# Performance work log

Measured on AMD Instinct MI355X. Metric: run time of the kernel, lower is better.

The kernel has to match this reference:

```python
import jax, jax.numpy as jnp
import numpy as np

B, T, D = 4, 1024, 256
H, DK, C = 8, 32, 16  # n_heads, d_key, pos-encoder hidden units
DV = D // H
NEG = -1e15
EPS_SM = 1e-5
EPS_LN = 1e-5
SLOPE = 0.01  # LeakyReLU default


def setup_inputs() -> dict:
    key = jax.random.key(0)
    ks = jax.random.split(key, 16)
    s = 0.05
    x = jax.random.normal(ks[0], (B, T, D), jnp.float32)
    src_mask = jax.random.randint(ks[1], (B, T, T), 0, 2).astype(bool)
    rel_dists = jax.random.uniform(ks[2], (B, 1, T, T), jnp.float32)
    Wq = jax.random.normal(ks[3], (H, DK, D), jnp.float32) * s
    Wk = jax.random.normal(ks[4], (H, DK, D), jnp.float32) * s
    Wv = jax.random.normal(ks[5], (H, DV, D), jnp.float32) * s
    pw1 = jax.random.normal(ks[6], (H, C), jnp.float32) * s
    pb1 = jax.random.normal(ks[7], (H, C), jnp.float32) * s
    pw2 = jax.random.normal(ks[8], (H, C), jnp.float32) * s
    pb2 = jax.random.normal(ks[9], (H,), jnp.float32) * s
    Wo = jax.random.normal(ks[10], (D, D), jnp.float32) * s
    bo = jax.random.normal(ks[11], (D,), jnp.float32) * s
    Wf = jax.random.normal(ks[12], (D, D), jnp.float32) * s
    bf = jax.random.normal(ks[13], (D,), jnp.float32) * s
    g1 = jnp.ones((D,), jnp.float32)
    beta1 = jnp.zeros((D,), jnp.float32)
    g2 = jnp.ones((D,), jnp.float32)
    beta2 = jnp.zeros((D,), jnp.float32)
    return dict(x=x, src_mask=src_mask, rel_dists=rel_dists, Wq=Wq, Wk=Wk, Wv=Wv,
                pw1=pw1, pb1=pb1, pw2=pw2, pb2=pb2, Wo=Wo, bo=bo, Wf=Wf, bf=bf,
                g1=g1, beta1=beta1, g2=g2, beta2=beta2)


def _l2norm(v):
    # F.normalize(p=2, dim=-1): v / max(||v||, 1e-12)
    n = jnp.sqrt(jnp.sum(v * v, axis=-1, keepdims=True))
    return v / jnp.maximum(n, 1e-12)


def _lrelu(h):
    return jnp.where(h >= 0, h, SLOPE * h)


def _pos_bias(d, pw1, pb1, pw2, pb2):
    # d: [B,T,T]; per-head 1x1-conv MLP applied elementwise.
    # Loop over the tiny channel dim (16) to avoid a [B,H,T,T,C] intermediate.
    bias = jnp.broadcast_to(pb2[None, :, None, None], (d.shape[0], pw1.shape[0], d.shape[1], d.shape[2]))
    for c in range(pw1.shape[1]):
        h = d[:, None] * pw1[None, :, c, None, None] + pb1[None, :, c, None, None]
        bias = bias + pw2[None, :, c, None, None] * _lrelu(h)
    return bias  # [B,H,T,T]


def _layer_norm(v, g, b):
    mu = jnp.mean(v, axis=-1, keepdims=True)
    var = jnp.mean((v - mu) ** 2, axis=-1, keepdims=True)
    return (v - mu) * jax.lax.rsqrt(var + EPS_LN) * g + b


def reference(x, src_mask, rel_dists, Wq, Wk, Wv, pw1, pb1, pw2, pb2,
              Wo, bo, Wf, bf, g1, beta1, g2, beta2):
    # cosine-normalized multi-head attention (all heads batched)
    q = _l2norm(jnp.einsum('btd,hkd->bhtk', x, Wq))
    k = _l2norm(jnp.einsum('bsd,hkd->bhsk', x, Wk))
    v = jnp.einsum('bsd,hvd->bhsv', x, Wv)
    logits = jnp.einsum('bhtk,bhsk->bhts', q, k)
    logits = logits - _pos_bias(rel_dists[:, 0], pw1, pb1, pw2, pb2)
    logits = jnp.where(src_mask[:, None], NEG, logits)
    # custom softmax: exp / (sum + 1e-5) (handles all-padded rows)
    z = jnp.exp(logits)
    attn = z / (jnp.sum(z, axis=-1, keepdims=True) + EPS_SM)
    heads = jnp.einsum('bhts,bhsv->bhtv', attn, v)
    y = heads.transpose(0, 2, 1, 3).reshape(x.shape[0], x.shape[1], -1)  # concat heads
    y = y @ Wo.T + bo
    # residual + LN + FFN (dropout is identity in eval mode)
    zz = _layer_norm(x + y, g1, beta1)
    z_ff = _lrelu(zz @ Wf.T + bf)
    return _layer_norm(zz + z_ff, g2, beta2)
```

## Files before the change

### kernel.cpp

```cpp
#include <hip/hip_runtime.h>
#include <math.h>

#define Bc 4
#define Tc 1024
#define Dc 256
#define Hc 8
#define Cc 16
#define LUTN 256
#define LOG2E 1.4426950408889634f

typedef __attribute__((ext_vector_type(8))) short short8;
typedef __attribute__((ext_vector_type(4))) float f32x4;

__device__ __forceinline__ unsigned bf16u(float x) {
    unsigned u = __float_as_uint(x);
    return (u + 0x7FFFu + ((u >> 16) & 1u)) >> 16;
}
__device__ __forceinline__ unsigned pk2(float lo, float hi) {
    return bf16u(lo) | (bf16u(hi) << 16);
}
__device__ __forceinline__ unsigned pk2t(float lo, float hi) {
    return __builtin_amdgcn_perm(__float_as_uint(hi), __float_as_uint(lo), 0x07060302u);
}
__device__ __forceinline__ float upk(unsigned v) { return __uint_as_float(v << 16); }
__device__ __forceinline__ float upkh(unsigned v) { return __uint_as_float(v & 0xffff0000u); }
__device__ __forceinline__ float fexp2(float x) { return __builtin_amdgcn_exp2f(x); }

__global__ __launch_bounds__(256) void prep_all(
    const float* __restrict__ x,
    const float* __restrict__ Wq, const float* __restrict__ Wk,
    const float* __restrict__ Wv, const float* __restrict__ Wo,
    const float* __restrict__ Wf,
    const float* __restrict__ rel, const int* __restrict__ msk,
    const float* __restrict__ pw1, const float* __restrict__ pb1,
    const float* __restrict__ pw2, const float* __restrict__ pb2,
    ushort* __restrict__ Xc, ushort* __restrict__ Wqkvc,
    ushort* __restrict__ Woc, ushort* __restrict__ Wfc,
    ushort* __restrict__ Dm, ushort* __restrict__ LUTb)
{
    const int bid = blockIdx.x;
    if (bid < 1344) {
        const int e = (bid * 256 + threadIdx.x) * 4;
        const float* src; ushort* dst; int off;
        if (e < 1048576)      { src = x;  dst = Xc;             off = e; }
        else if (e < 1114112) { src = Wq; dst = Wqkvc;          off = e - 1048576; }
        else if (e < 1179648) { src = Wk; dst = Wqkvc + 65536;  off = e - 1114112; }
        else if (e < 1245184) { src = Wv; dst = Wqkvc + 131072; off = e - 1179648; }
        else if (e < 1310720) { src = Wo; dst = Woc;            off = e - 1245184; }
        else                  { src = Wf; dst = Wfc;            off = e - 1310720; }
        float4 v = *(const float4*)(src + off);
        uint2 p; p.x = pk2(v.x, v.y); p.y = pk2(v.z, v.w);
        *(uint2*)(dst + off) = p;
    } else if (bid < 3392) {
        const size_t e = ((size_t)(bid - 1344) * 256 + threadIdx.x) * 8;
        float4 d0 = *(const float4*)(rel + e);
        float4 d1 = *(const float4*)(rel + e + 4);
        int4 m0 = *(const int4*)(msk + e);
        int4 m1 = *(const int4*)(msk + e + 4);
        uint4 o;
        o.x = pk2(m0.x ? -1.f : d0.x, m0.y ? -1.f : d0.y);
        o.y = pk2(m0.z ? -1.f : d0.z, m0.w ? -1.f : d0.w);
        o.z = pk2(m1.x ? -1.f : d1.x, m1.y ? -1.f : d1.y);
        o.w = pk2(m1.z ? -1.f : d1.z, m1.w ? -1.f : d1.w);
        *(uint4*)(Dm + e) = o;
    } else {
        const int bin = threadIdx.x;
        const float d0 = bin * (1.f / LUTN), d1 = (bin + 1) * (1.f / LUTN);
        for (int h = 0; h < Hc; ++h) {
            float y0 = pb2[h], y1 = pb2[h];
#pragma unroll
            for (int c = 0; c < Cc; ++c) {
                float w1 = pw1[h * Cc + c], b1 = pb1[h * Cc + c], w2 = pw2[h * Cc + c];
                float h0 = fmaf(w1, d0, b1), h1 = fmaf(w1, d1, b1);
                y0 = fmaf(w2, h0 >= 0.f ? h0 : 0.01f * h0, y0);
                y1 = fmaf(w2, h1 >= 0.f ? h1 : 0.01f * h1, y1);
            }
            float a = (y1 - y0) * (float)LUTN;
            float b = y0 - a * d0;
            LUTb[(h >> 2) * 2048 + bin * 8 + (h & 3) * 2]     = (ushort)bf16u(a * LOG2E);
            LUTb[(h >> 2) * 2048 + bin * 8 + (h & 3) * 2 + 1] = (ushort)bf16u(b * LOG2E);
        }
    }
}

__global__ __launch_bounds__(256) void qkv_direct(
    const ushort* __restrict__ Xc, const ushort* __restrict__ Wqkv,
    ushort* __restrict__ Qb, ushort* __restrict__ Kb, ushort* __restrict__ Vt)
{
    const int tid = threadIdx.x;
    const int w = tid >> 6;
    const int l = tid & 63;
    const int u = l & 15, g = l >> 4;
    const int rbase = blockIdx.x * 16;
    const int cb = (blockIdx.y * 4 + w) * 64;
    const int mat = cb >> 8;
    const int fcb = cb & 255;

    f32x4 acc[4];
#pragma unroll
    for (int nt = 0; nt < 4; ++nt) acc[nt] = (f32x4){0.f, 0.f, 0.f, 0.f};

    const ushort* arow = Xc + (size_t)(rbase + u) * 256 + g * 8;
#pragma unroll 2
    for (int k0 = 0; k0 < 256; k0 += 32) {
        short8 af = *(const short8*)(arow + k0);
#pragma unroll
        for (int nt = 0; nt < 4; ++nt) {
            short8 bfr = *(const short8*)(Wqkv + (size_t)(cb + nt * 16 + u) * 256 + k0 + g * 8);
            acc[nt] = __builtin_amdgcn_mfma_f32_16x16x32_bf16(af, bfr, acc[nt], 0, 0, 0);
        }
    }

    if (mat < 2) {
        ushort* Out = (mat == 0) ? Qb : Kb;
        const float post = (mat == 0) ? LOG2E : 1.f;
#pragma unroll
        for (int hp = 0; hp < 2; ++hp) {
            const int head = (fcb >> 5) + hp;
#pragma unroll
            for (int reg = 0; reg < 4; ++reg) {
                float ss = acc[2 * hp][reg] * acc[2 * hp][reg]
                         + acc[2 * hp + 1][reg] * acc[2 * hp + 1][reg];
                ss += __shfl_xor(ss, 1, 64);
                ss += __shfl_xor(ss, 2, 64);
                ss += __shfl_xor(ss, 4, 64);
                ss += __shfl_xor(ss, 8, 64);
                float scn = post / fmaxf(sqrtf(ss), 1e-12f);
                const int t = rbase + 4 * g + reg;
                const int bb = t >> 10, tt = t & 1023;
                const size_t base = ((size_t)(bb * 8 + head) * Tc + tt) * 32;
                Out[base + u]      = (ushort)bf16u(acc[2 * hp][reg] * scn);
                Out[base + 16 + u] = (ushort)bf16u(acc[2 * hp + 1][reg] * scn);
            }
        }
    } else {
#pragma unroll
        for (int nt = 0; nt < 4; ++nt) {
            const int head = (fcb >> 5) + (nt >> 1);
            const int vt = nt & 1;
#pragma unroll
            for (int reg = 0; reg < 4; ++reg) {
                const int s = rbase + 4 * g + reg;
                const int bb = s >> 10, ss = s & 1023;
                const int bh = bb * 8 + head;
                Vt[(((size_t)bh * 32 + (ss >> 5)) * 2 + vt) * 512 + u * 32 + (ss & 31)] =
                    (ushort)bf16u(acc[nt][reg]);
            }
        }
    }
}

__global__ __launch_bounds__(512) void attn_mfma(
    const ushort* __restrict__ Qb, const ushort* __restrict__ Kb,
    const ushort* __restrict__ Vt,
    const ushort* __restrict__ Dm, const ushort* __restrict__ LUTb,
    ushort* __restrict__ Yb)
{
    const int tid = threadIdx.x;
    const int w = tid >> 6;
    const int l = tid & 63;
    const int u = l & 15;
    const int g = l >> 4;
    const int t0 = blockIdx.x * 16;
    const int b = blockIdx.y;
    const int hg = blockIdx.z;

    __shared__ __align__(16) ushort lut_s[2048];
    __shared__ __align__(16) unsigned plds[8 * 320];
    __shared__ __align__(16) ushort comb[8 * 16 * 136];
    __shared__ float rs_s[8 * 64];

    *(uint2*)(lut_s + tid * 4) = *(const uint2*)(LUTb + hg * 2048 + tid * 4);

    const int bh0 = b * 8 + hg * 4;
    short8 qf[4];
#pragma unroll
    for (int hi = 0; hi < 4; ++hi)
        qf[hi] = *(const short8*)(Qb + (((size_t)(bh0 + hi) * Tc + t0 + u) * 32 + g * 8));

    const short8 ones = (short8){0x3F80, 0x3F80, 0x3F80, 0x3F80,
                                 0x3F80, 0x3F80, 0x3F80, 0x3F80};

    f32x4 oacc[4][2];
    f32x4 rsacc[4];
#pragma unroll
    for (int hi = 0; hi < 4; ++hi) {
        oacc[hi][0] = (f32x4){0.f, 0.f, 0.f, 0.f};
        oacc[hi][1] = (f32x4){0.f, 0.f, 0.f, 0.f};
        rsacc[hi]   = (f32x4){0.f, 0.f, 0.f, 0.f};
    }

    unsigned* pwb = plds + w * 320;
    const size_t dbase = (size_t)b * Tc * Tc;

    __syncthreads();

    const int s_begin = w * 128;
#pragma unroll
    for (int ch = 0; ch < 4; ++ch) {
        const int sc = s_begin + ch * 32;
        float dA[4], dB[4];
#pragma unroll
        for (int reg = 0; reg < 4; ++reg) {
            const int t = t0 + 4 * g + reg;
            unsigned dm = *(const unsigned*)(Dm + dbase + (size_t)t * Tc + sc + 2 * u);
            dA[reg] = upk(dm);
            dB[reg] = upkh(dm);
        }
        float biasA[4][4], biasB[4][4];
#pragma unroll
        for (int reg = 0; reg < 4; ++reg) {
            int iA = (int)(dA[reg] * (float)LUTN);
            int iB = (int)(dB[reg] * (float)LUTN);
            iA = iA < 0 ? 0 : (iA > LUTN - 1 ? LUTN - 1 : iA);
            iB = iB < 0 ? 0 : (iB > LUTN - 1 ? LUTN - 1 : iB);
            uint4 wA = *(const uint4*)(lut_s + iA * 8);
            uint4 wB = *(const uint4*)(lut_s + iB * 8);
            biasA[reg][0] = fmaf(upk(wA.x), dA[reg], upkh(wA.x));
            biasA[reg][1] = fmaf(upk(wA.y), dA[reg], upkh(wA.y));
            biasA[reg][2] = fmaf(upk(wA.z), dA[reg], upkh(wA.z));
            biasA[reg][3] = fmaf(upk(wA.w), dA[reg], upkh(wA.w));
            biasB[reg][0] = fmaf(upk(wB.x), dB[reg], upkh(wB.x));
            biasB[reg][1] = fmaf(upk(wB.y), dB[reg], upkh(wB.y));
            biasB[reg][2] = fmaf(upk(wB.z), dB[reg], upkh(wB.z));
            biasB[reg][3] = fmaf(upk(wB.w), dB[reg], upkh(wB.w));
        }
#pragma unroll
        for (int hi = 0; hi < 4; ++hi) {
            const size_t kb = ((size_t)(bh0 + hi) * Tc + sc + 2 * u) * 32 + g * 8;
            short8 kfA = *(const short8*)(Kb + kb);
            short8 kfB = *(const short8*)(Kb + kb + 32);
            const f32x4 z4 = (f32x4){0.f, 0.f, 0.f, 0.f};
            f32x4 sA = __builtin_amdgcn_mfma_f32_16x16x32_bf16(qf[hi], kfA, z4, 0, 0, 0);
            f32x4 sB = __builtin_amdgcn_mfma_f32_16x16x32_bf16(qf[hi], kfB, z4, 0, 0, 0);
#pragma unroll
            for (int reg = 0; reg < 4; ++reg) {
                float zA = (dA[reg] < 0.f) ? 0.f : fexp2(sA[reg] - biasA[reg][hi]);
                float zB = (dB[reg] < 0.f) ? 0.f : fexp2(sB[reg] - biasB[reg][hi]);
                pwb[(4 * g + reg) * 20 + u] = pk2t(zA, zB);
            }
            short8 pf = *(const short8*)((const char*)pwb + u * 80 + g * 16);
            const ushort* vb = Vt + ((size_t)(bh0 + hi) * 32 + (sc >> 5)) * 1024;
            short8 vf0 = *(const short8*)(vb + u * 32 + g * 8);
            short8 vf1 = *(const short8*)(vb + 512 + u * 32 + g * 8);
            oacc[hi][0] = __builtin_amdgcn_mfma_f32_16x16x32_bf16(pf, vf0, oacc[hi][0], 0, 0, 0);
            oacc[hi][1] = __builtin_amdgcn_mfma_f32_16x16x32_bf16(pf, vf1, oacc[hi][1], 0, 0, 0);
            rsacc[hi]   = __builtin_amdgcn_mfma_f32_16x16x32_bf16(pf, ones, rsacc[hi], 0, 0, 0);
        }
    }

#pragma unroll
    for (int hi = 0; hi < 4; ++hi)
        if (u == 0) {
#pragma unroll
            for (int reg = 0; reg < 4; ++reg)
                rs_s[(w * 4 + hi) * 16 + 4 * g + reg] = rsacc[hi][reg];
        }
#pragma unroll
    for (int hi = 0; hi < 4; ++hi)
#pragma unroll
        for (int vt = 0; vt < 2; ++vt)
#pragma unroll
            for (int reg = 0; reg < 4; ++reg)
                comb[w * 2176 + (4 * g + reg) * 136 + hi * 32 + vt * 16 + u] =
                    (ushort)(__float_as_uint(oacc[hi][vt][reg]) >> 16);
    __syncthreads();

    const int tl = tid >> 5;
    const int f0 = (tid & 31) * 4;
    const int hl = f0 >> 5;
    float rstot = 0.f;
#pragma unroll
    for (int ww = 0; ww < 8; ++ww) rstot += rs_s[(ww * 4 + hl) * 16 + tl];
    float inv = 1.f / (rstot + 1e-5f);
    float o[4] = {0.f, 0.f, 0.f, 0.f};
#pragma unroll
    for (int ww = 0; ww < 8; ++ww) {
        uint2 pv = *(const uint2*)&comb[ww * 2176 + tl * 136 + f0];
        o[0] += upk(pv.x); o[1] += upkh(pv.x);
        o[2] += upk(pv.y); o[3] += upkh(pv.y);
    }
    uint2 pw;
    pw.x = pk2(o[0] * inv, o[1] * inv);
    pw.y = pk2(o[2] * inv, o[3] * inv);
    *(uint2*)(Yb + ((size_t)b * Tc + t0 + tl) * Dc + hg * 128 + f0) = pw;
}

__global__ __launch_bounds__(256) void gemm_ln(
    const ushort* __restrict__ A, const ushort* __restrict__ W,
    const float* __restrict__ bias,
    const float* __restrict__ resF, const ushort* __restrict__ resB,
    const float* __restrict__ gam, const float* __restrict__ bet,
    float* __restrict__ outF, ushort* __restrict__ outB, int act)
{
    const int tid = threadIdx.x;
    const int w = tid >> 6;
    const int l = tid & 63;
    const int u = l & 15, g = l >> 4;
    const int rbase = blockIdx.x * 16;

    __shared__ float red1[64], red2[64];

    f32x4 acc[4];
#pragma unroll
    for (int nt = 0; nt < 4; ++nt) acc[nt] = (f32x4){0.f, 0.f, 0.f, 0.f};

    const ushort* arow = A + (size_t)(rbase + u) * 256 + g * 8;
#pragma unroll 2
    for (int k0 = 0; k0 < 256; k0 += 32) {
        short8 af = *(const short8*)(arow + k0);
#pragma unroll
        for (int nt = 0; nt < 4; ++nt) {
            short8 bfr = *(const short8*)(W + (size_t)(w * 64 + nt * 16 + u) * 256 + k0 + g * 8);
            acc[nt] = __builtin_amdgcn_mfma_f32_16x16x32_bf16(af, bfr, acc[nt], 0, 0, 0);
        }
    }

    float bv[4];
#pragma unroll
    for (int nt = 0; nt < 4; ++nt) bv[nt] = bias[w * 64 + nt * 16 + u];

    float sv[4][4];
#pragma unroll
    for (int reg = 0; reg < 4; ++reg) {
        const int row = rbase + 4 * g + reg;
        float s1 = 0.f, s2 = 0.f;
#pragma unroll
        for (int nt = 0; nt < 4; ++nt) {
            const int col = w * 64 + nt * 16 + u;
            float v = acc[nt][reg] + bv[nt];
            if (act) v = v >= 0.f ? v : 0.01f * v;
            float res = resF ? resF[(size_t)row * 256 + col]
                             : upk((unsigned)resB[(size_t)row * 256 + col]);
            float s = v + res;
            sv[reg][nt] = s;
            s1 += s;
            s2 = fmaf(s, s, s2);
        }
        s1 += __shfl_xor(s1, 1, 64); s2 += __shfl_xor(s2, 1, 64);
        s1 += __shfl_xor(s1, 2, 64); s2 += __shfl_xor(s2, 2, 64);
        s1 += __shfl_xor(s1, 4, 64); s2 += __shfl_xor(s2, 4, 64);
        s1 += __shfl_xor(s1, 8, 64); s2 += __shfl_xor(s2, 8, 64);
        if (u == 0) { red1[w * 16 + 4 * g + reg] = s1; red2[w * 16 + 4 * g + reg] = s2; }
    }
    __syncthreads();

    float gv[4], btv[4];
#pragma unroll
    for (int nt = 0; nt < 4; ++nt) {
        gv[nt]  = gam[w * 64 + nt * 16 + u];
        btv[nt] = bet[w * 64 + nt * 16 + u];
    }
#pragma unroll
    for (int reg = 0; reg < 4; ++reg) {
        const int row = rbase + 4 * g + reg;
        const int rl = 4 * g + reg;
        float S1 = red1[rl] + red1[16 + rl] + red1[32 + rl] + red1[48 + rl];
        float S2 = red2[rl] + red2[16 + rl] + red2[32 + rl] + red2[48 + rl];
        float mu = S1 * (1.f / 256.f);
        float var = S2 * (1.f / 256.f) - mu * mu;
        float rsig = rsqrtf(var + 1e-5f);
#pragma unroll
        for (int nt = 0; nt < 4; ++nt) {
            const int col = w * 64 + nt * 16 + u;
            float o = (sv[reg][nt] - mu) * rsig * gv[nt] + btv[nt];
            if (outF) outF[(size_t)row * 256 + col] = o;
            else      outB[(size_t)row * 256 + col] = (ushort)bf16u(o);
        }
    }
}

extern "C" void kernel_launch(void* const* d_in, const int* in_sizes, int n_in,
                              void* d_out, int out_size, void* d_ws, size_t ws_size,
                              hipStream_t stream) {
    const float* x    = (const float*)d_in[0];
    const int*   mask = (const int*)d_in[1];
    const float* rel  = (const float*)d_in[2];
    const float* Wq   = (const float*)d_in[3];
    const float* Wk   = (const float*)d_in[4];
    const float* Wv   = (const float*)d_in[5];
    const float* pw1  = (const float*)d_in[6];
    const float* pb1  = (const float*)d_in[7];
    const float* pw2  = (const float*)d_in[8];
    const float* pb2  = (const float*)d_in[9];
    const float* Wo   = (const float*)d_in[10];
    const float* bo   = (const float*)d_in[11];
    const float* Wf   = (const float*)d_in[12];
    const float* bf   = (const float*)d_in[13];
    const float* g1   = (const float*)d_in[14];
    const float* be1  = (const float*)d_in[15];
    const float* g2   = (const float*)d_in[16];
    const float* be2  = (const float*)d_in[17];
    float* out = (float*)d_out;

    char* wsb = (char*)d_ws;
    ushort* Xc    = (ushort*)(wsb);
    ushort* Qb    = (ushort*)(wsb + (size_t)( 2 << 20));
    ushort* Kb    = (ushort*)(wsb + (size_t)( 4 << 20));
    ushort* Vt    = (ushort*)(wsb + (size_t)( 6 << 20));
    ushort* Yb    = (ushort*)(wsb + (size_t)( 8 << 20));
    ushort* Wqkvc = (ushort*)(wsb + (size_t)(10 << 20));
    ushort* Woc   = (ushort*)(wsb + (size_t)(10 << 20) + (512 << 10));
    ushort* Wfc   = (ushort*)(wsb + (size_t)(10 << 20) + (768 << 10));
    ushort* LUTb  = (ushort*)(wsb + (size_t)(11 << 20));
    ushort* ZZb   = (ushort*)(wsb + (size_t)(12 << 20));
    ushort* Dm    = (ushort*)(wsb + (size_t)(16 << 20));

    prep_all<<<3393, 256, 0, stream>>>(x, Wq, Wk, Wv, Wo, Wf, rel, mask,
                                       pw1, pb1, pw2, pb2,
                                       Xc, Wqkvc, Woc, Wfc, Dm, LUTb);
    qkv_direct<<<dim3(256, 3), 256, 0, stream>>>(Xc, Wqkvc, Qb, Kb, Vt);
    attn_mfma<<<dim3(64, 4, 2), 512, 0, stream>>>(Qb, Kb, Vt, Dm, LUTb, Yb);
    gemm_ln<<<256, 256, 0, stream>>>(Yb, Woc, bo, x, nullptr, g1, be1,
                                     nullptr, ZZb, 0);
    gemm_ln<<<256, 256, 0, stream>>>(ZZb, Wfc, bf, nullptr, ZZb, g2, be2,
                                     out, nullptr, 1);
}
```

Baseline: 177.8 us.

## Co-schedule mask/distance packing with QKV GEMM and widen LN GEMM blocks

Splits the prep kernel so that only the bf16 casts run first, and folds the rel-dist/mask packing and LUT build into the QKV projection launch as extra blocks. The bandwidth-heavy mask conversion then overlaps with the QKV MFMA work instead of running serially before it. The gemm_ln kernels move to 512 threads with 8 waves each covering 32 columns, which adds parallelism per row tile and changes the LayerNorm reduction to sum over 8 wave partials. The cost is more waves competing for the same row data in each block.

```diff
diff --git a/kernel.cpp b/kernel.cpp
--- a/kernel.cpp
+++ b/kernel.cpp
@@ -26,33 +26,57 @@
 __device__ __forceinline__ float upkh(unsigned v) { return __uint_as_float(v & 0xffff0000u); }
 __device__ __forceinline__ float fexp2(float x) { return __builtin_amdgcn_exp2f(x); }
 
-__global__ __launch_bounds__(256) void prep_all(
+__global__ __launch_bounds__(256) void prep_cast(
     const float* __restrict__ x,
     const float* __restrict__ Wq, const float* __restrict__ Wk,
     const float* __restrict__ Wv, const float* __restrict__ Wo,
     const float* __restrict__ Wf,
+    ushort* __restrict__ Xc, ushort* __restrict__ Wqkvc,
+    ushort* __restrict__ Woc, ushort* __restrict__ Wfc)
+{
+    const int e = (blockIdx.x * 256 + threadIdx.x) * 4;
+    const float* src; ushort* dst; int off;
+    if (e < 1048576)      { src = x;  dst = Xc;             off = e; }
+    else if (e < 1114112) { src = Wq; dst = Wqkvc;          off = e - 1048576; }
+    else if (e < 1179648) { src = Wk; dst = Wqkvc + 65536;  off = e - 1114112; }
+    else if (e < 1245184) { src = Wv; dst = Wqkvc + 131072; off = e - 1179648; }
+    else if (e < 1310720) { src = Wo; dst = Woc;            off = e - 1245184; }
+    else                  { src = Wf; dst = Wfc;            off = e - 1310720; }
+    float4 v = *(const float4*)(src + off);
+    uint2 p; p.x = pk2(v.x, v.y); p.y = pk2(v.z, v.w);
+    *(uint2*)(dst + off) = p;
+}
+
+__global__ __launch_bounds__(256) void qkv_fused(
+    const ushort* __restrict__ Xc, const ushort* __restrict__ Wqkv,
     const float* __restrict__ rel, const int* __restrict__ msk,
     const float* __restrict__ pw1, const float* __restrict__ pb1,
     const float* __restrict__ pw2, const float* __restrict__ pb2,
-    ushort* __restrict__ Xc, ushort* __restrict__ Wqkvc,
-    ushort* __restrict__ Woc, ushort* __restrict__ Wfc,
+    ushort* __restrict__ Qb, ushort* __restrict__ Kb, ushort* __restrict__ Vt,
     ushort* __restrict__ Dm, ushort* __restrict__ LUTb)
 {
     const int bid = blockIdx.x;
-    if (bid < 1344) {
-        const int e = (bid * 256 + threadIdx.x) * 4;
-        const float* src; ushort* dst; int off;
-        if (e < 1048576)      { src = x;  dst = Xc;             off = e; }
-        else if (e < 1114112) { src = Wq; dst = Wqkvc;          off = e - 1048576; }
-        else if (e < 1179648) { src = Wk; dst = Wqkvc + 65536;  off = e - 1114112; }
-        else if (e < 1245184) { src = Wv; dst = Wqkvc + 131072; off = e - 1179648; }
-        else if (e < 1310720) { src = Wo; dst = Woc;            off = e - 1245184; }
-        else                  { src = Wf; dst = Wfc;            off = e - 1310720; }
-        float4 v = *(const float4*)(src + off);
-        uint2 p; p.x = pk2(v.x, v.y); p.y = pk2(v.z, v.w);
-        *(uint2*)(dst + off) = p;
-    } else if (bid < 3392) {
-        const size_t e = ((size_t)(bid - 1344) * 256 + threadIdx.x) * 8;
+    if (bid >= 768) {
+        if (bid == 2816) {
+            const int bin = threadIdx.x;
+            const float d0 = bin * (1.f / LUTN), d1 = (bin + 1) * (1.f / LUTN);
+            for (int h = 0; h < Hc; ++h) {
+                float y0 = pb2[h], y1 = pb2[h];
+#pragma unroll
+                for (int c = 0; c < Cc; ++c) {
+                    float w1 = pw1[h * Cc + c], b1 = pb1[h * Cc + c], w2 = pw2[h * Cc + c];
+                    float h0 = fmaf(w1, d0, b1), h1 = fmaf(w1, d1, b1);
+                    y0 = fmaf(w2, h0 >= 0.f ? h0 : 0.01f * h0, y0);
+                    y1 = fmaf(w2, h1 >= 0.f ? h1 : 0.01f * h1, y1);
+                }
+                float a = (y1 - y0) * (float)LUTN;
+                float b = y0 - a * d0;
+                LUTb[(h >> 2) * 2048 + bin * 8 + (h & 3) * 2]     = (ushort)bf16u(a * LOG2E);
+                LUTb[(h >> 2) * 2048 + bin * 8 + (h & 3) * 2 + 1] = (ushort)bf16u(b * LOG2E);
+            }
+            return;
+        }
+        const size_t e = ((size_t)(bid - 768) * 256 + threadIdx.x) * 8;
         float4 d0 = *(const float4*)(rel + e);
         float4 d1 = *(const float4*)(rel + e + 4);
         int4 m0 = *(const int4*)(msk + e);
@@ -63,36 +87,15 @@
         o.z = pk2(m1.x ? -1.f : d1.x, m1.y ? -1.f : d1.y);
         o.w = pk2(m1.z ? -1.f : d1.z, m1.w ? -1.f : d1.w);
         *(uint4*)(Dm + e) = o;
-    } else {
-        const int bin = threadIdx.x;
-        const float d0 = bin * (1.f / LUTN), d1 = (bin + 1) * (1.f / LUTN);
-        for (int h = 0; h < Hc; ++h) {
-            float y0 = pb2[h], y1 = pb2[h];
-#pragma unroll
-            for (int c = 0; c < Cc; ++c) {
-                float w1 = pw1[h * Cc + c], b1 = pb1[h * Cc + c], w2 = pw2[h * Cc + c];
-                float h0 = fmaf(w1, d0, b1), h1 = fmaf(w1, d1, b1);
-                y0 = fmaf(w2, h0 >= 0.f ? h0 : 0.01f * h0, y0);
-                y1 = fmaf(w2, h1 >= 0.f ? h1 : 0.01f * h1, y1);
-            }
-            float a = (y1 - y0) * (float)LUTN;
-            float b = y0 - a * d0;
-            LUTb[(h >> 2) * 2048 + bin * 8 + (h & 3) * 2]     = (ushort)bf16u(a * LOG2E);
-            LUTb[(h >> 2) * 2048 + bin * 8 + (h & 3) * 2 + 1] = (ushort)bf16u(b * LOG2E);
-        }
-    }
-}
-
-__global__ __launch_bounds__(256) void qkv_direct(
-    const ushort* __restrict__ Xc, const ushort* __restrict__ Wqkv,
-    ushort* __restrict__ Qb, ushort* __restrict__ Kb, ushort* __restrict__ Vt)
-{
+        return;
+    }
+
     const int tid = threadIdx.x;
     const int w = tid >> 6;
     const int l = tid & 63;
     const int u = l & 15, g = l >> 4;
-    const int rbase = blockIdx.x * 16;
-    const int cb = (blockIdx.y * 4 + w) * 64;
+    const int rbase = (bid & 255) * 16;
+    const int cb = ((bid >> 8) * 4 + w) * 64;
     const int mat = cb >> 8;
     const int fcb = cb & 255;
 
@@ -286,7 +289,7 @@
     *(uint2*)(Yb + ((size_t)b * Tc + t0 + tl) * Dc + hg * 128 + f0) = pw;
 }
 
-__global__ __launch_bounds__(256) void gemm_ln(
+__global__ __launch_bounds__(512) void gemm_ln(
     const ushort* __restrict__ A, const ushort* __restrict__ W,
     const float* __restrict__ bias,
     const float* __restrict__ resF, const ushort* __restrict__ resB,
@@ -299,35 +302,35 @@
     const int u = l & 15, g = l >> 4;
     const int rbase = blockIdx.x * 16;
 
-    __shared__ float red1[64], red2[64];
-
-    f32x4 acc[4];
-#pragma unroll
-    for (int nt = 0; nt < 4; ++nt) acc[nt] = (f32x4){0.f, 0.f, 0.f, 0.f};
+    __shared__ float red1[128], red2[128];
+
+    f32x4 acc[2];
+#pragma unroll
+    for (int nt = 0; nt < 2; ++nt) acc[nt] = (f32x4){0.f, 0.f, 0.f, 0.f};
 
     const ushort* arow = A + (size_t)(rbase + u) * 256 + g * 8;
 #pragma unroll 2
     for (int k0 = 0; k0 < 256; k0 += 32) {
         short8 af = *(const short8*)(arow + k0);
 #pragma unroll
-        for (int nt = 0; nt < 4; ++nt) {
-            short8 bfr = *(const short8*)(W + (size_t)(w * 64 + nt * 16 + u) * 256 + k0 + g * 8);
+        for (int nt = 0; nt < 2; ++nt) {
+            short8 bfr = *(const short8*)(W + (size_t)(w * 32 + nt * 16 + u) * 256 + k0 + g * 8);
             acc[nt] = __builtin_amdgcn_mfma_f32_16x16x32_bf16(af, bfr, acc[nt], 0, 0, 0);
         }
     }
 
-    float bv[4];
-#pragma unroll
-    for (int nt = 0; nt < 4; ++nt) bv[nt] = bias[w * 64 + nt * 16 + u];
-
-    float sv[4][4];
+    float bv[2];
+#pragma unroll
+    for (int nt = 0; nt < 2; ++nt) bv[nt] = bias[w * 32 + nt * 16 + u];
+
+    float sv[4][2];
 #pragma unroll
     for (int reg = 0; reg < 4; ++reg) {
         const int row = rbase + 4 * g + reg;
         float s1 = 0.f, s2 = 0.f;
 #pragma unroll
-        for (int nt = 0; nt < 4; ++nt) {
-            const int col = w * 64 + nt * 16 + u;
+        for (int nt = 0; nt < 2; ++nt) {
+            const int col = w * 32 + nt * 16 + u;
             float v = acc[nt][reg] + bv[nt];
             if (act) v = v >= 0.f ? v : 0.01f * v;
             float res = resF ? resF[(size_t)row * 256 + col]
@@ -345,24 +348,25 @@
     }
     __syncthreads();
 
-    float gv[4], btv[4];
-#pragma unroll
-    for (int nt = 0; nt < 4; ++nt) {
-        gv[nt]  = gam[w * 64 + nt * 16 + u];
-        btv[nt] = bet[w * 64 + nt * 16 + u];
+    float gv[2], btv[2];
+#pragma unroll
+    for (int nt = 0; nt < 2; ++nt) {
+        gv[nt]  = gam[w * 32 + nt * 16 + u];
+        btv[nt] = bet[w * 32 + nt * 16 + u];
     }
 #pragma unroll
     for (int reg = 0; reg < 4; ++reg) {
         const int row = rbase + 4 * g + reg;
         const int rl = 4 * g + reg;
-        float S1 = red1[rl] + red1[16 + rl] + red1[32 + rl] + red1[48 + rl];
-        float S2 = red2[rl] + red2[16 + rl] + red2[32 + rl] + red2[48 + rl];
+        float S1 = 0.f, S2 = 0.f;
+#pragma unroll
+        for (int ww = 0; ww < 8; ++ww) { S1 += red1[ww * 16 + rl]; S2 += red2[ww * 16 + rl]; }
         float mu = S1 * (1.f / 256.f);
         float var = S2 * (1.f / 256.f) - mu * mu;
         float rsig = rsqrtf(var + 1e-5f);
 #pragma unroll
-        for (int nt = 0; nt < 4; ++nt) {
-            const int col = w * 64 + nt * 16 + u;
+        for (int nt = 0; nt < 2; ++nt) {
+            const int col = w * 32 + nt * 16 + u;
             float o = (sv[reg][nt] - mu) * rsig * gv[nt] + btv[nt];
             if (outF) outF[(size_t)row * 256 + col] = o;
             else      outB[(size_t)row * 256 + col] = (ushort)bf16u(o);
@@ -406,13 +410,14 @@
     ushort* ZZb   = (ushort*)(wsb + (size_t)(12 << 20));
     ushort* Dm    = (ushort*)(wsb + (size_t)(16 << 20));
 
-    prep_all<<<3393, 256, 0, stream>>>(x, Wq, Wk, Wv, Wo, Wf, rel, mask,
-                                       pw1, pb1, pw2, pb2,
-                                       Xc, Wqkvc, Woc, Wfc, Dm, LUTb);
-    qkv_direct<<<dim3(256, 3), 256, 0, stream>>>(Xc, Wqkvc, Qb, Kb, Vt);
+    prep_cast<<<1344, 256, 0, stream>>>(x, Wq, Wk, Wv, Wo, Wf,
+                                        Xc, Wqkvc, Woc, Wfc);
+    qkv_fused<<<2817, 256, 0, stream>>>(Xc, Wqkvc, rel, mask,
+                                        pw1, pb1, pw2, pb2,
+                                        Qb, Kb, Vt, Dm, LUTb);
     attn_mfma<<<dim3(64, 4, 2), 512, 0, stream>>>(Qb, Kb, Vt, Dm, LUTb, Yb);
-    gemm_ln<<<256, 256, 0, stream>>>(Yb, Woc, bo, x, nullptr, g1, be1,
+    gemm_ln<<<256, 512, 0, stream>>>(Yb, Woc, bo, x, nullptr, g1, be1,
                                      nullptr, ZZb, 0);
-    gemm_ln<<<256, 256, 0, stream>>>(ZZb, Wfc, bf, nullptr, ZZb, g2, be2,
+    gemm_ln<<<256, 512, 0, stream>>>(ZZb, Wfc, bf, nullptr, ZZb, g2, be2,
                                      out, nullptr, 1);
 }
```

After: 177.8 us. No clear change (-0.0%).
